# Performance work log

Hardware: AMD Instinct MI355X
Metric: run time of the kernel (lower is better)

Reference implementation:

```python
import jax, jax.numpy as jnp
import numpy as np

B, T, N, F_IN, F_OUT, H = 32, 32, 256, 32, 32, 256
NEG_SLOPE = 0.2  # GATConv default leaky-relu slope


def setup_inputs() -> dict:
    key = jax.random.key(0)
    ks = jax.random.split(key, 12)
    x = jax.random.normal(ks[0], (B, T, N, F_IN), dtype=jnp.float32)
    u = jax.random.uniform(ks[1], (B, T, N, N))
    w = jax.random.uniform(ks[2], (B, T, N, N))
    adj = jnp.where(u < 0.1, w, 0.0).astype(jnp.float32)
    # GAT params (heads=1, concat=False)
    W = jax.random.normal(ks[3], (F_IN, F_OUT), dtype=jnp.float32) / np.sqrt(F_IN)
    a_src = jax.random.normal(ks[4], (F_OUT,), dtype=jnp.float32) / np.sqrt(F_OUT)
    a_dst = jax.random.normal(ks[5], (F_OUT,), dtype=jnp.float32) / np.sqrt(F_OUT)
    gat_b = jnp.zeros((F_OUT,), dtype=jnp.float32)
    # LSTM params (PyTorch layout, gate order i,f,g,o)
    IN = N * F_OUT
    s = 1.0 / np.sqrt(H)
    W_ih = jax.random.uniform(ks[6], (4 * H, IN), minval=-s, maxval=s, dtype=jnp.float32)
    W_hh = jax.random.uniform(ks[7], (4 * H, H), minval=-s, maxval=s, dtype=jnp.float32)
    b_ih = jax.random.uniform(ks[8], (4 * H,), minval=-s, maxval=s, dtype=jnp.float32)
    b_hh = jax.random.uniform(ks[9], (4 * H,), minval=-s, maxval=s, dtype=jnp.float32)
    # output Linear
    Wo = jax.random.uniform(ks[10], (N, H), minval=-s, maxval=s, dtype=jnp.float32)
    bo = jax.random.uniform(ks[11], (N,), minval=-s, maxval=s, dtype=jnp.float32)
    return {"x": x, "adj": adj, "W": W, "a_src": a_src, "a_dst": a_dst,
            "gat_b": gat_b, "W_ih": W_ih, "W_hh": W_hh, "b_ih": b_ih,
            "b_hh": b_hh, "Wo": Wo, "bo": bo}


def _gat(x, adj, W, a_src, a_dst, gat_b):
    # batched over (B,T). h: [B,T,N,F_OUT]
    h = jnp.einsum('btnf,fo->btno', x, W)
    s_src = jnp.einsum('btno,o->btn', h, a_src)  # contribution of source node j
    s_dst = jnp.einsum('btno,o->btn', h, a_dst)  # contribution of target node i
    # e[i,j] = LeakyReLU(a_dst.h_i + a_src.h_j)
    e = jax.nn.leaky_relu(s_dst[..., :, None] + s_src[..., None, :], NEG_SLOPE)
    # edge (row=j -> col=i) exists iff adj[j,i] != 0; GATConv adds self-loops
    mask = (jnp.swapaxes(adj, -1, -2) != 0) | jnp.eye(N, dtype=bool)
    alpha = jax.nn.softmax(jnp.where(mask, e, -jnp.inf), axis=-1)  # softmax over sources j per target i
    return jnp.einsum('btij,btjo->btio', alpha, h) + gat_b


def _lstm_last(seq, W_ih, W_hh, b_ih, b_hh):
    # seq: [B,T,IN] -> last hidden state [B,H]
    def step(carry, x_t):
        h_prev, c_prev = carry
        gates = x_t @ W_ih.T + h_prev @ W_hh.T + (b_ih + b_hh)
        i, f, g, o = jnp.split(gates, 4, axis=-1)
        c = jax.nn.sigmoid(f) * c_prev + jax.nn.sigmoid(i) * jnp.tanh(g)
        h = jax.nn.sigmoid(o) * jnp.tanh(c)
        return (h, c), None
    init = (jnp.zeros((seq.shape[0], H), seq.dtype), jnp.zeros((seq.shape[0], H), seq.dtype))
    (h_last, _), _ = jax.lax.scan(step, init, jnp.swapaxes(seq, 0, 1))
    return h_last


def reference(x, adj, W, a_src, a_dst, gat_b, W_ih, W_hh, b_ih, b_hh, Wo, bo):
    gat_out = _gat(x, adj, W, a_src, a_dst, gat_b)            # [B,T,N,F_OUT]
    seq = gat_out.reshape(gat_out.shape[0], gat_out.shape[1], -1)  # [B,T,N*F_OUT]
    h_last = _lstm_last(seq, W_ih, W_hh, b_ih, b_hh)          # [B,H]
    return h_last @ Wo.T + bo                                  # [B,N]
```

## Files before the change

kernel.cpp:

```cpp
#include <hip/hip_runtime.h>
#include <cstdint>

constexpr int B_ = 32, T_ = 32, N_ = 256, FIN = 32, FOUT = 32, H_ = 256;
constexpr int IN_ = N_ * FOUT;
constexpr int G4  = 4 * H_;
constexpr int BT  = B_ * T_;
#define NEG_SLOPE 0.2f

typedef _Float16 half8 __attribute__((ext_vector_type(8)));
typedef _Float16 h2    __attribute__((ext_vector_type(2)));
typedef float    f4    __attribute__((ext_vector_type(4)));

__device__ inline uint32_t pkh2(float a, float b) {
    union { uint32_t u; _Float16 h[2]; } z;
    z.h[0] = (_Float16)a; z.h[1] = (_Float16)b; return z.u;
}
__device__ inline float f16lo(uint32_t u){ union{uint32_t u; _Float16 h[2];} z; z.u=u; return (float)z.h[0]; }
__device__ inline float f16hi(uint32_t u){ union{uint32_t u; _Float16 h[2];} z; z.u=u; return (float)z.h[1]; }

__device__ inline float dot2f(uint32_t w, uint32_t h, float acc) {
    union { uint32_t u; h2 v; } a, b; a.u = w; b.u = h;
#if __has_builtin(__builtin_amdgcn_fdot2)
    return __builtin_amdgcn_fdot2(a.v, b.v, acc, false);
#else
    return acc + (float)a.v.x * (float)b.v.x + (float)a.v.y * (float)b.v.y;
#endif
}

__device__ inline void gload16(const void* g, void* l) {
    __builtin_amdgcn_global_load_lds(
        (const __attribute__((address_space(1))) void*)g,
        (__attribute__((address_space(3))) void*)l, 16, 0, 0);
}

__global__ __launch_bounds__(256) void gat_kernel(
    const float* __restrict__ x, const float* __restrict__ adj,
    const float* __restrict__ W, const float* __restrict__ a_src,
    const float* __restrict__ a_dst, const float* __restrict__ gat_b,
    _Float16* __restrict__ seq)
{
    const int bt = blockIdx.x;
    const int i  = threadIdx.x;
    __shared__ float Ws[FIN * FOUT];
    __shared__ __align__(16) uint32_t hpp[128 * 36];
    __shared__ float ssrc[N_];
    __shared__ float asv[FOUT], adv[FOUT], gbv[FOUT];

    for (int t = i; t < FIN * FOUT; t += 256) Ws[t] = W[t];
    if (i < FOUT) { asv[i] = a_src[i]; adv[i] = a_dst[i]; gbv[i] = gat_b[i]; }

    float xr[FIN];
    const float* xrow = x + ((size_t)bt * N_ + i) * FIN;
    #pragma unroll
    for (int f4i = 0; f4i < FIN / 4; ++f4i) {
        float4 v = reinterpret_cast<const float4*>(xrow)[f4i];
        xr[4*f4i] = v.x; xr[4*f4i+1] = v.y; xr[4*f4i+2] = v.z; xr[4*f4i+3] = v.w;
    }
    __syncthreads();

    float hr[FOUT];
    #pragma unroll
    for (int k4 = 0; k4 < FOUT / 4; ++k4) {
        float ax = 0.f, ay = 0.f, az = 0.f, aw = 0.f;
        #pragma unroll
        for (int f = 0; f < FIN; ++f) {
            float4 w4 = *reinterpret_cast<const float4*>(&Ws[f*FOUT + 4*k4]);
            ax += xr[f]*w4.x; ay += xr[f]*w4.y; az += xr[f]*w4.z; aw += xr[f]*w4.w;
        }
        hr[4*k4] = ax; hr[4*k4+1] = ay; hr[4*k4+2] = az; hr[4*k4+3] = aw;
    }
    float ss = 0.f, sd = 0.f;
    #pragma unroll
    for (int k = 0; k < FOUT; ++k) { ss += hr[k]*asv[k]; sd += hr[k]*adv[k]; }
    _Float16* hp16 = reinterpret_cast<_Float16*>(hpp);
    #pragma unroll
    for (int k = 0; k < FOUT; ++k)
        hp16[(i >> 1) * 72 + 2*k + (i & 1)] = (_Float16)hr[k];
    ssrc[i] = ss;
    __syncthreads();

    float acc[FOUT];
    #pragma unroll
    for (int k = 0; k < FOUT; ++k) acc[k] = 0.f;
    float l = 0.f;
    const float* adjcol = adj + (size_t)bt * N_ * N_ + i;
    #pragma unroll 2
    for (int q = 0; q < 128; ++q) {
        const int j0 = 2*q, j1 = 2*q + 1;
        float a0 = adjcol[(size_t)j0 * N_];
        float a1 = adjcol[(size_t)j1 * N_];
        float e0 = sd + ssrc[j0]; e0 = e0 > 0.f ? e0 : NEG_SLOPE * e0;
        float e1 = sd + ssrc[j1]; e1 = e1 > 0.f ? e1 : NEG_SLOPE * e1;
        float p0 = ((a0 != 0.f) || (j0 == i)) ? __expf(e0) : 0.f;
        float p1 = ((a1 != 0.f) || (j1 == i)) ? __expf(e1) : 0.f;
        l += p0 + p1;
        uint32_t pk = pkh2(p0, p1);
        const uint32_t* hq = &hpp[q * 36];
        #pragma unroll
        for (int k4 = 0; k4 < 8; ++k4) {
            uint4 hv = *reinterpret_cast<const uint4*>(&hq[4*k4]);
            acc[4*k4+0] = dot2f(pk, hv.x, acc[4*k4+0]);
            acc[4*k4+1] = dot2f(pk, hv.y, acc[4*k4+1]);
            acc[4*k4+2] = dot2f(pk, hv.z, acc[4*k4+2]);
            acc[4*k4+3] = dot2f(pk, hv.w, acc[4*k4+3]);
        }
    }
    float inv = 1.f / l;
    _Float16 vh[FOUT];
    #pragma unroll
    for (int k = 0; k < FOUT; ++k)
        vh[k] = (_Float16)(acc[k]*inv + gbv[k]);
    _Float16* orow = seq + (size_t)bt * IN_ + i * FOUT;
    #pragma unroll
    for (int k8 = 0; k8 < FOUT/8; ++k8)
        *reinterpret_cast<half8*>(orow + 8*k8) = *reinterpret_cast<half8*>(&vh[8*k8]);
}

__global__ __launch_bounds__(256) void pack_wih_kernel(
    const float* __restrict__ Wih, _Float16* __restrict__ out)
{
    int idx = (blockIdx.x * 256 + threadIdx.x) * 8;
    float4 v0 = *reinterpret_cast<const float4*>(Wih + idx);
    float4 v1 = *reinterpret_cast<const float4*>(Wih + idx + 4);
    half8 o;
    o[0]=(_Float16)v0.x; o[1]=(_Float16)v0.y; o[2]=(_Float16)v0.z; o[3]=(_Float16)v0.w;
    o[4]=(_Float16)v1.x; o[5]=(_Float16)v1.y; o[6]=(_Float16)v1.z; o[7]=(_Float16)v1.w;
    *reinterpret_cast<half8*>(out + idx) = o;
}

__global__ __launch_bounds__(256) void pack_whh_kernel(
    const float* __restrict__ Whh, uint32_t* __restrict__ pwv,
    uint32_t* __restrict__ pwl, uint32_t* __restrict__ pws)
{
    int g = blockIdx.x * 256 + threadIdx.x;
    const float* row = Whh + (size_t)g * H_;
    #pragma unroll
    for (int p = 0; p < 128; ++p) {
        float2 v = *reinterpret_cast<const float2*>(row + 2*p);
        uint32_t u = pkh2(v.x, v.y);
        if (p < 64) pwv[p * 1024 + g] = u;
        else if (p < 88) { int pp = p - 64; pwl[(pp >> 2) * 4096 + g * 4 + (pp & 3)] = u; }
        else            { int pp = p - 88; pws[(pp >> 2) * 4096 + g * 4 + (pp & 3)] = u; }
    }
}

__global__ __launch_bounds__(256, 4) void gemm_kernel(
    const _Float16* __restrict__ A, const _Float16* __restrict__ Bh,
    float* __restrict__ G)
{
    __shared__ __align__(16) _Float16 As[128 * 32];
    __shared__ __align__(16) _Float16 Bs[128 * 32];
    const int t = threadIdx.x;
    const int L = t & 63, w = t >> 6;
    const int wm = w & 1, wn = w >> 1;
    const int m0 = blockIdx.y * 128, n0 = blockIdx.x * 128;
    const int kz = blockIdx.z * 1024;

    f4 acc[4][4] = {};
    const int q0 = t, q1 = t + 256;
    const int row0 = q0 >> 2, kc0 = q0 & 3;
    const int row1 = q1 >> 2, kc1 = q1 & 3;
    const int la = (L & 15) * 32 + (L >> 4) * 8;

    const _Float16* A0 = A + (size_t)(m0 + row0) * IN_ + kz + kc0 * 8;
    const _Float16* A1 = A + (size_t)(m0 + row1) * IN_ + kz + kc1 * 8;
    const _Float16* B0 = Bh + (size_t)(n0 + row0) * IN_ + kz + kc0 * 8;
    const _Float16* B1 = Bh + (size_t)(n0 + row1) * IN_ + kz + kc1 * 8;
    for (int kb = 0; kb < 1024; kb += 32) {
        __syncthreads();
        gload16(A0 + kb, &As[q0 * 8]);
        gload16(A1 + kb, &As[q1 * 8]);
        gload16(B0 + kb, &Bs[q0 * 8]);
        gload16(B1 + kb, &Bs[q1 * 8]);
        __syncthreads();
        half8 af[4], bf[4];
        #pragma unroll
        for (int mi = 0; mi < 4; ++mi)
            af[mi] = *reinterpret_cast<const half8*>(&As[(wm*64 + mi*16) * 32 + la]);
        #pragma unroll
        for (int ni = 0; ni < 4; ++ni)
            bf[ni] = *reinterpret_cast<const half8*>(&Bs[(wn*64 + ni*16) * 32 + la]);
        #pragma unroll
        for (int mi = 0; mi < 4; ++mi)
            #pragma unroll
            for (int ni = 0; ni < 4; ++ni)
                acc[mi][ni] = __builtin_amdgcn_mfma_f32_16x16x32_f16(
                    af[mi], bf[ni], acc[mi][ni], 0, 0, 0);
    }
    const int cn = n0 + wn * 64 + (L & 15);
    const int rm = m0 + wm * 64 + (L >> 4) * 4;
    #pragma unroll
    for (int mi = 0; mi < 4; ++mi)
        #pragma unroll
        for (int ni = 0; ni < 4; ++ni)
            #pragma unroll
            for (int r = 0; r < 4; ++r)
                atomicAdd(&G[(size_t)(rm + mi*16 + r) * G4 + cn + ni*16], acc[mi][ni][r]);
}

__global__ __launch_bounds__(1024) void lstm_kernel(
    const float* __restrict__ G, const uint32_t* __restrict__ pwv,
    const uint32_t* __restrict__ pwl, const uint32_t* __restrict__ pws,
    const float* __restrict__ b_ih, const float* __restrict__ b_hh,
    const float* __restrict__ Wo, const float* __restrict__ bo,
    float* __restrict__ out)
{
    const int b = blockIdx.x;
    const int g = threadIdx.x;
    __shared__ __align__(16) uint32_t hsp[128];
    __shared__ float gsh[G4];
    __shared__ __align__(16) uint32_t wl[6 * 4096];

    uint32_t wv[64];
    #pragma unroll
    for (int p = 0; p < 64; ++p) wv[p] = pwv[p * 1024 + g];
    {
        const uint4* s = reinterpret_cast<const uint4*>(pwl);
        uint4* d = reinterpret_cast<uint4*>(wl);
        #pragma unroll
        for (int r = 0; r < 6; ++r) d[r * 1024 + g] = s[r * 1024 + g];
    }
    if (g < 128) hsp[g] = 0u;
    float c = 0.f;
    const float bias = b_ih[g] + b_hh[g];
    const float* Gb = G + (size_t)b * T_ * G4 + g;
    const uint4* pws4 = reinterpret_cast<const uint4*>(pws);
    const uint4* wl4  = reinterpret_cast<const uint4*>(wl);
    const uint4* hsp4 = reinterpret_cast<const uint4*>(hsp);
    float gnext = Gb[0];
    __syncthreads();

    for (int t = 0; t < T_; ++t) {
        float acc = bias + gnext;
        if (t + 1 < T_) gnext = Gb[(size_t)(t + 1) * G4];
        #pragma unroll
        for (int q = 0; q < 32; ++q) {
            uint4 h4 = hsp4[q];
            uint4 w4;
            if (q < 16) {
                w4.x = wv[4*q]; w4.y = wv[4*q+1]; w4.z = wv[4*q+2]; w4.w = wv[4*q+3];
            } else if (q < 22) {
                w4 = wl4[(q - 16) * 1024 + g];
            } else {
                w4 = pws4[(q - 22) * 1024 + g];
            }
            acc = dot2f(w4.x, h4.x, acc);
            acc = dot2f(w4.y, h4.y, acc);
            acc = dot2f(w4.z, h4.z, acc);
            acc = dot2f(w4.w, h4.w, acc);
        }
        gsh[g] = acc;
        __syncthreads();
        if (g < H_) {
            float xi = gsh[g], xf = gsh[H_ + g], xg = gsh[2*H_ + g], xo = gsh[3*H_ + g];
            float si = 1.f / (1.f + __expf(-xi));
            float sf = 1.f / (1.f + __expf(-xf));
            float so = 1.f / (1.f + __expf(-xo));
            float eg = __expf(2.f * xg);
            float tg = 1.f - 2.f / (eg + 1.f);
            c = sf * c + si * tg;
            float ec = __expf(2.f * c);
            float th = 1.f - 2.f / (ec + 1.f);
            reinterpret_cast<_Float16*>(hsp)[g] = (_Float16)(so * th);
        }
        __syncthreads();
    }
    if (g < N_) {
        const float* worow = Wo + (size_t)g * H_;
        float o = bo[g];
        #pragma unroll
        for (int q = 0; q < 32; ++q) {
            uint4 hq = hsp4[q];
            float4 w0 = *reinterpret_cast<const float4*>(worow + q*8);
            float4 w1 = *reinterpret_cast<const float4*>(worow + q*8 + 4);
            o += w0.x * f16lo(hq.x) + w0.y * f16hi(hq.x)
               + w0.z * f16lo(hq.y) + w0.w * f16hi(hq.y)
               + w1.x * f16lo(hq.z) + w1.y * f16hi(hq.z)
               + w1.z * f16lo(hq.w) + w1.w * f16hi(hq.w);
        }
        out[(size_t)b * N_ + g] = o;
    }
}

extern "C" void kernel_launch(void* const* d_in, const int* in_sizes, int n_in,
                              void* d_out, int out_size, void* d_ws, size_t ws_size,
                              hipStream_t stream) {
    const float* x     = (const float*)d_in[0];
    const float* adj   = (const float*)d_in[1];
    const float* W     = (const float*)d_in[2];
    const float* a_src = (const float*)d_in[3];
    const float* a_dst = (const float*)d_in[4];
    const float* gat_b = (const float*)d_in[5];
    const float* W_ih  = (const float*)d_in[6];
    const float* W_hh  = (const float*)d_in[7];
    const float* b_ih  = (const float*)d_in[8];
    const float* b_hh  = (const float*)d_in[9];
    const float* Wo    = (const float*)d_in[10];
    const float* bo    = (const float*)d_in[11];
    float* out = (float*)d_out;

    _Float16* seq   = (_Float16*)d_ws;
    _Float16* wih_h = seq + (size_t)BT * IN_;
    float*    G     = (float*)(wih_h + (size_t)G4 * IN_);
    uint32_t* pwv   = (uint32_t*)(G + (size_t)BT * G4);
    uint32_t* pwl   = pwv + 64 * 1024;
    uint32_t* pws   = pwl + 24 * 1024;

    hipMemsetAsync(G, 0, (size_t)BT * G4 * sizeof(float), stream);
    pack_whh_kernel<<<dim3(4), dim3(256), 0, stream>>>(W_hh, pwv, pwl, pws);
    pack_wih_kernel<<<dim3(4096), dim3(256), 0, stream>>>(W_ih, wih_h);
    gat_kernel<<<dim3(BT), dim3(256), 0, stream>>>(x, adj, W, a_src, a_dst, gat_b, seq);
    gemm_kernel<<<dim3(8, 8, 8), dim3(256), 0, stream>>>(seq, wih_h, G);
    lstm_kernel<<<dim3(B_), dim3(1024), 0, stream>>>(G, pwv, pwl, pws, b_ih, b_hh, Wo, bo, out);
}
```

Measured before the change: 612.3 us.

## Use MFMA for GAT aggregation and move more W_hh rows into LDS

The GAT attention aggregation is rewritten. Each thread writes its unnormalized attention probabilities for a 64-source chunk into a swizzled LDS tile, and the alpha·h product is then computed with 16x16x32 f16 MFMA instructions instead of per-thread dot2 loops over 32 accumulators. This cuts VALU work and register pressure, at the cost of extra LDS traffic and a different output write pattern that uses scalar half stores. Separately, the LSTM kernel keeps 8 instead of 6 blocks of packed recurrent weights in LDS, which reduces the per-step global loads of W_hh.

```diff
diff --git a/kernel.cpp b/kernel.cpp
--- a/kernel.cpp
+++ b/kernel.cpp
@@ -10,6 +10,8 @@
 typedef _Float16 half8 __attribute__((ext_vector_type(8)));
 typedef _Float16 h2    __attribute__((ext_vector_type(2)));
 typedef float    f4    __attribute__((ext_vector_type(4)));
+
+union U48 { uint4 u; half8 h; };
 
 __device__ inline uint32_t pkh2(float a, float b) {
     union { uint32_t u; _Float16 h[2]; } z;
@@ -41,9 +43,12 @@
 {
     const int bt = blockIdx.x;
     const int i  = threadIdx.x;
+    const int L  = i & 63, w = i >> 6;
     __shared__ float Ws[FIN * FOUT];
-    __shared__ __align__(16) uint32_t hpp[128 * 36];
+    __shared__ __align__(16) _Float16 hT[32 * 264];
+    __shared__ __align__(16) uint32_t Pc[256 * 36];
     __shared__ float ssrc[N_];
+    __shared__ float linv[N_];
     __shared__ float asv[FOUT], adv[FOUT], gbv[FOUT];
 
     for (int t = i; t < FIN * FOUT; t += 256) Ws[t] = W[t];
@@ -72,48 +77,63 @@
     float ss = 0.f, sd = 0.f;
     #pragma unroll
     for (int k = 0; k < FOUT; ++k) { ss += hr[k]*asv[k]; sd += hr[k]*adv[k]; }
-    _Float16* hp16 = reinterpret_cast<_Float16*>(hpp);
-    #pragma unroll
-    for (int k = 0; k < FOUT; ++k)
-        hp16[(i >> 1) * 72 + 2*k + (i & 1)] = (_Float16)hr[k];
+    #pragma unroll
+    for (int k = 0; k < FOUT; ++k) hT[k*264 + i] = (_Float16)hr[k];
     ssrc[i] = ss;
     __syncthreads();
 
-    float acc[FOUT];
-    #pragma unroll
-    for (int k = 0; k < FOUT; ++k) acc[k] = 0.f;
     float l = 0.f;
+    f4 acc[4][2] = {};
     const float* adjcol = adj + (size_t)bt * N_ * N_ + i;
-    #pragma unroll 2
-    for (int q = 0; q < 128; ++q) {
-        const int j0 = 2*q, j1 = 2*q + 1;
-        float a0 = adjcol[(size_t)j0 * N_];
-        float a1 = adjcol[(size_t)j1 * N_];
-        float e0 = sd + ssrc[j0]; e0 = e0 > 0.f ? e0 : NEG_SLOPE * e0;
-        float e1 = sd + ssrc[j1]; e1 = e1 > 0.f ? e1 : NEG_SLOPE * e1;
-        float p0 = ((a0 != 0.f) || (j0 == i)) ? __expf(e0) : 0.f;
-        float p1 = ((a1 != 0.f) || (j1 == i)) ? __expf(e1) : 0.f;
-        l += p0 + p1;
-        uint32_t pk = pkh2(p0, p1);
-        const uint32_t* hq = &hpp[q * 36];
-        #pragma unroll
-        for (int k4 = 0; k4 < 8; ++k4) {
-            uint4 hv = *reinterpret_cast<const uint4*>(&hq[4*k4]);
-            acc[4*k4+0] = dot2f(pk, hv.x, acc[4*k4+0]);
-            acc[4*k4+1] = dot2f(pk, hv.y, acc[4*k4+1]);
-            acc[4*k4+2] = dot2f(pk, hv.z, acc[4*k4+2]);
-            acc[4*k4+3] = dot2f(pk, hv.w, acc[4*k4+3]);
-        }
-    }
-    float inv = 1.f / l;
-    _Float16 vh[FOUT];
-    #pragma unroll
-    for (int k = 0; k < FOUT; ++k)
-        vh[k] = (_Float16)(acc[k]*inv + gbv[k]);
-    _Float16* orow = seq + (size_t)bt * IN_ + i * FOUT;
-    #pragma unroll
-    for (int k8 = 0; k8 < FOUT/8; ++k8)
-        *reinterpret_cast<half8*>(orow + 8*k8) = *reinterpret_cast<half8*>(&vh[8*k8]);
+    const int key = (i >> 3) & 3;
+    const int m = L & 15, G = L >> 4;
+
+    for (int c = 0; c < 4; ++c) {
+        const int j0 = c * 64;
+        #pragma unroll 8
+        for (int q = 0; q < 32; ++q) {
+            int ja = j0 + 2*q, jb = ja + 1;
+            float a0 = adjcol[(size_t)ja * N_];
+            float a1 = adjcol[(size_t)jb * N_];
+            float e0 = sd + ssrc[ja]; e0 = e0 > 0.f ? e0 : NEG_SLOPE * e0;
+            float e1 = sd + ssrc[jb]; e1 = e1 > 0.f ? e1 : NEG_SLOPE * e1;
+            float p0 = ((a0 != 0.f) || (ja == i)) ? __expf(e0) : 0.f;
+            float p1 = ((a1 != 0.f) || (jb == i)) ? __expf(e1) : 0.f;
+            l += p0 + p1;
+            Pc[i*36 + (((q >> 2) ^ key) << 2) + (q & 3)] = pkh2(p0, p1);
+        }
+        #pragma unroll
+        for (int ks = 0; ks < 2; ++ks) {
+            U48 b0, b1;
+            b0.h = *reinterpret_cast<const half8*>(&hT[m*264        + j0 + ks*32 + G*8]);
+            b1.h = *reinterpret_cast<const half8*>(&hT[(m+16)*264   + j0 + ks*32 + G*8]);
+            #pragma unroll
+            for (int it = 0; it < 4; ++it) {
+                int row = w*64 + it*16 + m;
+                int rkey = (row >> 3) & 3;
+                U48 a;
+                a.u = reinterpret_cast<const uint4*>(&Pc[row*36])[ks*4 + (G ^ rkey)];
+                acc[it][0] = __builtin_amdgcn_mfma_f32_16x16x32_f16(a.h, b0.h, acc[it][0], 0, 0, 0);
+                acc[it][1] = __builtin_amdgcn_mfma_f32_16x16x32_f16(a.h, b1.h, acc[it][1], 0, 0, 0);
+            }
+        }
+    }
+    linv[i] = 1.f / l;
+    _Float16* obase = seq + (size_t)bt * IN_;
+    #pragma unroll
+    for (int it = 0; it < 4; ++it) {
+        int ib = w*64 + it*16 + G*4;
+        #pragma unroll
+        for (int ot = 0; ot < 2; ++ot) {
+            int o = ot*16 + m;
+            float gb = gbv[o];
+            #pragma unroll
+            for (int r = 0; r < 4; ++r) {
+                int row = ib + r;
+                obase[row * FOUT + o] = (_Float16)(acc[it][ot][r] * linv[row] + gb);
+            }
+        }
+    }
 }
 
 __global__ __launch_bounds__(256) void pack_wih_kernel(
@@ -139,8 +159,8 @@
         float2 v = *reinterpret_cast<const float2*>(row + 2*p);
         uint32_t u = pkh2(v.x, v.y);
         if (p < 64) pwv[p * 1024 + g] = u;
-        else if (p < 88) { int pp = p - 64; pwl[(pp >> 2) * 4096 + g * 4 + (pp & 3)] = u; }
-        else            { int pp = p - 88; pws[(pp >> 2) * 4096 + g * 4 + (pp & 3)] = u; }
+        else if (p < 96) { int pp = p - 64; pwl[(pp >> 2) * 4096 + g * 4 + (pp & 3)] = u; }
+        else             { int pp = p - 96; pws[(pp >> 2) * 4096 + g * 4 + (pp & 3)] = u; }
     }
 }
 
@@ -209,7 +229,7 @@
     const int g = threadIdx.x;
     __shared__ __align__(16) uint32_t hsp[128];
     __shared__ float gsh[G4];
-    __shared__ __align__(16) uint32_t wl[6 * 4096];
+    __shared__ __align__(16) uint32_t wl[8 * 4096];
 
     uint32_t wv[64];
     #pragma unroll
@@ -218,7 +238,7 @@
         const uint4* s = reinterpret_cast<const uint4*>(pwl);
         uint4* d = reinterpret_cast<uint4*>(wl);
         #pragma unroll
-        for (int r = 0; r < 6; ++r) d[r * 1024 + g] = s[r * 1024 + g];
+        for (int r = 0; r < 8; ++r) d[r * 1024 + g] = s[r * 1024 + g];
     }
     if (g < 128) hsp[g] = 0u;
     float c = 0.f;
@@ -239,10 +259,10 @@
             uint4 w4;
             if (q < 16) {
                 w4.x = wv[4*q]; w4.y = wv[4*q+1]; w4.z = wv[4*q+2]; w4.w = wv[4*q+3];
-            } else if (q < 22) {
+            } else if (q < 24) {
                 w4 = wl4[(q - 16) * 1024 + g];
             } else {
-                w4 = pws4[(q - 22) * 1024 + g];
+                w4 = pws4[(q - 24) * 1024 + g];
             }
             acc = dot2f(w4.x, h4.x, acc);
             acc = dot2f(w4.y, h4.y, acc);
@@ -304,7 +324,7 @@
     float*    G     = (float*)(wih_h + (size_t)G4 * IN_);
     uint32_t* pwv   = (uint32_t*)(G + (size_t)BT * G4);
     uint32_t* pwl   = pwv + 64 * 1024;
-    uint32_t* pws   = pwl + 24 * 1024;
+    uint32_t* pws   = pwl + 32 * 1024;
 
     hipMemsetAsync(G, 0, (size_t)BT * G4 * sizeof(float), stream);
     pack_whh_kernel<<<dim3(4), dim3(256), 0, stream>>>(W_hh, pwv, pwl, pws);
```

After: 585.0 us. 4.5% less time.
